# Kernel optimization log

Measured on AMD Instinct MI355X. Metric: run time of the kernel, lower is better.

Reference implementation:

```python
import jax, jax.numpy as jnp
import numpy as np

MAX_ITER = 20
TAU = 1.0

def setup_inputs() -> dict:
    key = jax.random.key(0)
    s = jax.random.normal(key, (256, 512, 512), dtype=jnp.float32)
    return {"s": s}

def reference(s):
    # Sinkhorn-Knopp in log space. With nrows=ncols=None and square input,
    # the per-batch loop in the original reduces to full-matrix normalization.
    # Even iterations normalize along the last axis (dim=1 of each 2D matrix),
    # odd iterations along the row axis.
    log_s = s / TAU
    for i in range(MAX_ITER):
        axis = 2 if i % 2 == 0 else 1
        log_s = log_s - jax.nn.logsumexp(log_s, axis=axis, keepdims=True)
    return jnp.exp(log_s)
```

## Files before the change

### kernel.cpp

```cpp
#include <hip/hip_runtime.h>

#define N 512
#define WAVES 16
#define BLOCK (WAVES * 64)
#define ROWS_PER_WAVE (N / WAVES)

__global__ __launch_bounds__(BLOCK, 1)
void sinkhorn_kernel(const float* __restrict__ A, float* __restrict__ Out) {
    __shared__ float sv[N];
    __shared__ float sev[N];
    __shared__ float su[N];
    __shared__ float spart[WAVES][N];

    const float* __restrict__ Ab = A + (size_t)blockIdx.x * N * N;
    float* __restrict__ Ob       = Out + (size_t)blockIdx.x * N * N;
    const int tid  = threadIdx.x;
    const int lane = tid & 63;
    const int wave = tid >> 6;

    if (tid < N) { sv[tid] = 0.0f; sev[tid] = 1.0f; }
    __syncthreads();

    for (int pass = 0; pass < 10; ++pass) {
        const float4 v0  = ((const float4*)sv)[lane];
        const float4 v1  = ((const float4*)sv)[lane + 64];
        const float4 ev0 = ((const float4*)sev)[lane];
        const float4 ev1 = ((const float4*)sev)[lane + 64];
        float t0=0.f,t1=0.f,t2=0.f,t3=0.f,t4=0.f,t5=0.f,t6=0.f,t7=0.f;

        #pragma unroll 2
        for (int k = 0; k < ROWS_PER_WAVE; ++k) {
            const int row = k * WAVES + wave;
            const float4* R = (const float4*)(Ab + (size_t)row * N);
            const float4 x0 = R[lane];
            const float4 x1 = R[lane + 64];

            const float e0 = __expf(x0.x - v0.x);
            const float e1 = __expf(x0.y - v0.y);
            const float e2 = __expf(x0.z - v0.z);
            const float e3 = __expf(x0.w - v0.w);
            const float e4 = __expf(x1.x - v1.x);
            const float e5 = __expf(x1.y - v1.y);
            const float e6 = __expf(x1.z - v1.z);
            const float e7 = __expf(x1.w - v1.w);

            float S = ((e0 + e1) + (e2 + e3)) + ((e4 + e5) + (e6 + e7));
            #pragma unroll
            for (int m = 1; m < 64; m <<= 1) S += __shfl_xor(S, m, 64);

            if (lane == 0) su[row] = __logf(S);
            const float inv = 1.0f / S;

            t0 += e0 * ev0.x * inv;
            t1 += e1 * ev0.y * inv;
            t2 += e2 * ev0.z * inv;
            t3 += e3 * ev0.w * inv;
            t4 += e4 * ev1.x * inv;
            t5 += e5 * ev1.y * inv;
            t6 += e6 * ev1.z * inv;
            t7 += e7 * ev1.w * inv;
        }

        ((float4*)spart[wave])[lane]      = make_float4(t0, t1, t2, t3);
        ((float4*)spart[wave])[lane + 64] = make_float4(t4, t5, t6, t7);
        __syncthreads();

        if (tid < N) {
            float s = 0.f;
            #pragma unroll
            for (int w = 0; w < WAVES; ++w) s += spart[w][tid];
            sev[tid] = s;
            sv[tid]  = __logf(s);
        }
        __syncthreads();
    }

    const float4 v0 = ((const float4*)sv)[lane];
    const float4 v1 = ((const float4*)sv)[lane + 64];
    #pragma unroll 2
    for (int k = 0; k < ROWS_PER_WAVE; ++k) {
        const int row = k * WAVES + wave;
        const float4* R = (const float4*)(Ab + (size_t)row * N);
        float4* W       = (float4*)(Ob + (size_t)row * N);
        const float4 x0 = R[lane];
        const float4 x1 = R[lane + 64];
        const float ui  = su[row];

        float4 o0, o1;
        o0.x = __expf(x0.x - ui - v0.x);
        o0.y = __expf(x0.y - ui - v0.y);
        o0.z = __expf(x0.z - ui - v0.z);
        o0.w = __expf(x0.w - ui - v0.w);
        o1.x = __expf(x1.x - ui - v1.x);
        o1.y = __expf(x1.y - ui - v1.y);
        o1.z = __expf(x1.z - ui - v1.z);
        o1.w = __expf(x1.w - ui - v1.w);

        W[lane]      = o0;
        W[lane + 64] = o1;
    }
}

extern "C" void kernel_launch(void* const* d_in, const int* in_sizes, int n_in,
                              void* d_out, int out_size, void* d_ws, size_t ws_size,
                              hipStream_t stream) {
    const float* s = (const float*)d_in[0];
    float* out = (float*)d_out;
    const int nmat = in_sizes[0] / (N * N);
    sinkhorn_kernel<<<nmat, BLOCK, 0, stream>>>(s, out);
}
```

Before: 780.2 us.

## Cache exp(A) in output buffer and run Sinkhorn in linear scaling space

Computes exp(A) once in the first pass and stores it into the output buffer, then runs the remaining passes as multiplicative row/column scaling of that cached matrix instead of recomputing exponentials of log-space values. This removes the per-element transcendental work from nine of the ten passes and from the final write, replacing it with multiplies and reciprocals. It adds a global write of the full matrix in the first pass. It also drops the max-subtraction safety of log space, so large input values could overflow, although the inputs here are standard normal. The unroll factor also rises from 2 to 4.

```diff
diff --git a/kernel.cpp b/kernel.cpp
--- a/kernel.cpp
+++ b/kernel.cpp
@@ -7,97 +7,119 @@
 
 __global__ __launch_bounds__(BLOCK, 1)
 void sinkhorn_kernel(const float* __restrict__ A, float* __restrict__ Out) {
-    __shared__ float sv[N];
-    __shared__ float sev[N];
-    __shared__ float su[N];
+    __shared__ float swv[N];
+    __shared__ float sinvS[N];
     __shared__ float spart[WAVES][N];
 
-    const float* __restrict__ Ab = A + (size_t)blockIdx.x * N * N;
-    float* __restrict__ Ob       = Out + (size_t)blockIdx.x * N * N;
+    const float* __restrict__ Ab = A   + (size_t)blockIdx.x * N * N;
+    float* __restrict__ Eb       = Out + (size_t)blockIdx.x * N * N;
     const int tid  = threadIdx.x;
     const int lane = tid & 63;
     const int wave = tid >> 6;
 
-    if (tid < N) { sv[tid] = 0.0f; sev[tid] = 1.0f; }
-    __syncthreads();
-
-    for (int pass = 0; pass < 10; ++pass) {
-        const float4 v0  = ((const float4*)sv)[lane];
-        const float4 v1  = ((const float4*)sv)[lane + 64];
-        const float4 ev0 = ((const float4*)sev)[lane];
-        const float4 ev1 = ((const float4*)sev)[lane + 64];
+    {
         float t0=0.f,t1=0.f,t2=0.f,t3=0.f,t4=0.f,t5=0.f,t6=0.f,t7=0.f;
-
-        #pragma unroll 2
+        #pragma unroll 4
         for (int k = 0; k < ROWS_PER_WAVE; ++k) {
             const int row = k * WAVES + wave;
             const float4* R = (const float4*)(Ab + (size_t)row * N);
+            float4*       W = (float4*)(Eb + (size_t)row * N);
             const float4 x0 = R[lane];
             const float4 x1 = R[lane + 64];
 
-            const float e0 = __expf(x0.x - v0.x);
-            const float e1 = __expf(x0.y - v0.y);
-            const float e2 = __expf(x0.z - v0.z);
-            const float e3 = __expf(x0.w - v0.w);
-            const float e4 = __expf(x1.x - v1.x);
-            const float e5 = __expf(x1.y - v1.y);
-            const float e6 = __expf(x1.z - v1.z);
-            const float e7 = __expf(x1.w - v1.w);
+            const float e0 = __expf(x0.x), e1 = __expf(x0.y),
+                        e2 = __expf(x0.z), e3 = __expf(x0.w);
+            const float e4 = __expf(x1.x), e5 = __expf(x1.y),
+                        e6 = __expf(x1.z), e7 = __expf(x1.w);
+
+            W[lane]      = make_float4(e0, e1, e2, e3);
+            W[lane + 64] = make_float4(e4, e5, e6, e7);
 
             float S = ((e0 + e1) + (e2 + e3)) + ((e4 + e5) + (e6 + e7));
             #pragma unroll
             for (int m = 1; m < 64; m <<= 1) S += __shfl_xor(S, m, 64);
 
-            if (lane == 0) su[row] = __logf(S);
             const float inv = 1.0f / S;
+            if (lane == 0) sinvS[row] = inv;
 
-            t0 += e0 * ev0.x * inv;
-            t1 += e1 * ev0.y * inv;
-            t2 += e2 * ev0.z * inv;
-            t3 += e3 * ev0.w * inv;
-            t4 += e4 * ev1.x * inv;
-            t5 += e5 * ev1.y * inv;
-            t6 += e6 * ev1.z * inv;
-            t7 += e7 * ev1.w * inv;
+            t0 += e0 * inv; t1 += e1 * inv; t2 += e2 * inv; t3 += e3 * inv;
+            t4 += e4 * inv; t5 += e5 * inv; t6 += e6 * inv; t7 += e7 * inv;
+        }
+        ((float4*)spart[wave])[lane]      = make_float4(t0, t1, t2, t3);
+        ((float4*)spart[wave])[lane + 64] = make_float4(t4, t5, t6, t7);
+        __syncthreads();
+        if (tid < N) {
+            float s = 0.f;
+            #pragma unroll
+            for (int w = 0; w < WAVES; ++w) s += spart[w][tid];
+            swv[tid] = 1.0f / s;
+        }
+        __syncthreads();
+    }
+
+    for (int pass = 1; pass < 10; ++pass) {
+        const float4 w0 = ((const float4*)swv)[lane];
+        const float4 w1 = ((const float4*)swv)[lane + 64];
+        float t0=0.f,t1=0.f,t2=0.f,t3=0.f,t4=0.f,t5=0.f,t6=0.f,t7=0.f;
+
+        #pragma unroll 4
+        for (int k = 0; k < ROWS_PER_WAVE; ++k) {
+            const int row = k * WAVES + wave;
+            const float4* R = (const float4*)(Eb + (size_t)row * N);
+            const float4 a0 = R[lane];
+            const float4 a1 = R[lane + 64];
+
+            const float s01 = a0.x * w0.x + a0.y * w0.y;
+            const float s23 = a0.z * w0.z + a0.w * w0.w;
+            const float s45 = a1.x * w1.x + a1.y * w1.y;
+            const float s67 = a1.z * w1.z + a1.w * w1.w;
+            float S = (s01 + s23) + (s45 + s67);
+            #pragma unroll
+            for (int m = 1; m < 64; m <<= 1) S += __shfl_xor(S, m, 64);
+
+            const float inv = 1.0f / S;
+            if (lane == 0) sinvS[row] = inv;
+
+            t0 += a0.x * inv; t1 += a0.y * inv; t2 += a0.z * inv; t3 += a0.w * inv;
+            t4 += a1.x * inv; t5 += a1.y * inv; t6 += a1.z * inv; t7 += a1.w * inv;
         }
 
         ((float4*)spart[wave])[lane]      = make_float4(t0, t1, t2, t3);
         ((float4*)spart[wave])[lane + 64] = make_float4(t4, t5, t6, t7);
         __syncthreads();
-
         if (tid < N) {
             float s = 0.f;
             #pragma unroll
             for (int w = 0; w < WAVES; ++w) s += spart[w][tid];
-            sev[tid] = s;
-            sv[tid]  = __logf(s);
+            swv[tid] = 1.0f / s;
         }
         __syncthreads();
     }
 
-    const float4 v0 = ((const float4*)sv)[lane];
-    const float4 v1 = ((const float4*)sv)[lane + 64];
-    #pragma unroll 2
-    for (int k = 0; k < ROWS_PER_WAVE; ++k) {
-        const int row = k * WAVES + wave;
-        const float4* R = (const float4*)(Ab + (size_t)row * N);
-        float4* W       = (float4*)(Ob + (size_t)row * N);
-        const float4 x0 = R[lane];
-        const float4 x1 = R[lane + 64];
-        const float ui  = su[row];
+    {
+        const float4 w0 = ((const float4*)swv)[lane];
+        const float4 w1 = ((const float4*)swv)[lane + 64];
+        #pragma unroll 4
+        for (int k = 0; k < ROWS_PER_WAVE; ++k) {
+            const int row = k * WAVES + wave;
+            float4* W = (float4*)(Eb + (size_t)row * N);
+            const float4 a0 = W[lane];
+            const float4 a1 = W[lane + 64];
+            const float c = sinvS[row];
 
-        float4 o0, o1;
-        o0.x = __expf(x0.x - ui - v0.x);
-        o0.y = __expf(x0.y - ui - v0.y);
-        o0.z = __expf(x0.z - ui - v0.z);
-        o0.w = __expf(x0.w - ui - v0.w);
-        o1.x = __expf(x1.x - ui - v1.x);
-        o1.y = __expf(x1.y - ui - v1.y);
-        o1.z = __expf(x1.z - ui - v1.z);
-        o1.w = __expf(x1.w - ui - v1.w);
+            float4 o0, o1;
+            o0.x = a0.x * (c * w0.x);
+            o0.y = a0.y * (c * w0.y);
+            o0.z = a0.z * (c * w0.z);
+            o0.w = a0.w * (c * w0.w);
+            o1.x = a1.x * (c * w1.x);
+            o1.y = a1.y * (c * w1.y);
+            o1.z = a1.z * (c * w1.z);
+            o1.w = a1.w * (c * w1.w);
 
-        W[lane]      = o0;
-        W[lane + 64] = o1;
+            W[lane]      = o0;
+            W[lane + 64] = o1;
+        }
     }
 }
 
```

Measured after the change: 825.5 us. 1.06x slower.
